# Optimization experiments

Measured on AMD Instinct MI355X. Metric: run time of the kernel, lower is better.

## Reference

```python
import jax, jax.numpy as jnp
import numpy as np

B, D_IN, N, K, L, D_OUT = 64, 1024, 50000, 32, 3, 256


def setup_inputs() -> dict:
    key = jax.random.key(0)
    k = jax.random.split(key, 7)
    x = jax.random.normal(k[0], (B, D_IN), dtype=jnp.float32)
    W0 = jax.random.normal(k[1], (N, D_IN), dtype=jnp.float32) * 0.02
    b0 = jax.random.normal(k[2], (N,), dtype=jnp.float32) * 0.02
    Wv = jax.random.normal(k[3], (L, N, K), dtype=jnp.float32) * 0.1
    Wout = jax.random.normal(k[4], (D_OUT, N), dtype=jnp.float32) * 0.02
    bout = jax.random.normal(k[5], (D_OUT,), dtype=jnp.float32) * 0.02
    src = jax.random.randint(k[6], (L, N, K), 0, N, dtype=jnp.int64)
    return {"x": x, "W0": W0, "b0": b0, "Wv": Wv, "Wout": Wout, "bout": bout, "src": src}


def reference(x, W0, b0, Wv, Wout, bout, src):
    # layer 0: dense input->sources, relu, transpose -> [N, B]
    h = jax.nn.relu(x @ W0.T + b0).T

    # each hidden layer: per-vertex gather of K source activations + 1xK matmul + relu
    def step(h_prev, layer):
        w, s = layer                      # w: [N, K], s: [N, K]
        gathered = h_prev[s]              # [N, K, B] irregular gather
        h_new = jax.nn.relu(jnp.einsum('nk,nkb->nb', w, gathered))
        return h_new, None

    h, _ = jax.lax.scan(step, h, (Wv, src))

    # last layer -> output Linear (the module's _linear_dummy)
    return h.T @ Wout.T + bout            # [B, D_OUT]
```

## Files before the change

### kernel.cpp

```cpp
#include <hip/hip_runtime.h>

#define NV 50000
#define NVP 50176
#define BDIM 64
#define DIN 1024
#define KFAN 32
#define DOUT 256
#define KSTEPS (DIN / 32)
#define OPC_CHUNK 128
#define OPC_NCH (NVP / OPC_CHUNK)

typedef short bf16x8 __attribute__((ext_vector_type(8)));
typedef float f32x4 __attribute__((ext_vector_type(4)));

__device__ __forceinline__ unsigned short bf16_rtn(float f) {
  unsigned u = __float_as_uint(f);
  return (unsigned short)((u + 0x7fffu + ((u >> 16) & 1u)) >> 16);
}
__device__ __forceinline__ float bf16_to_f(unsigned short v) {
  return __uint_as_float(((unsigned)v) << 16);
}

__global__ __launch_bounds__(256) void pack_x(const float* __restrict__ x,
                                              uint4* __restrict__ xpk) {
  int tid = blockIdx.x * 256 + threadIdx.x;
  int ks = tid >> 8;
  int g = (tid >> 6) & 3;
  int l = tid & 63;
  int b = g * 16 + (l & 15);
  int k0 = ks * 32 + (l >> 4) * 8;
  unsigned hi[8], lo[8];
#pragma unroll
  for (int j = 0; j < 8; ++j) {
    float f = x[b * DIN + k0 + j];
    unsigned u = __float_as_uint(f);
    hi[j] = u >> 16;
    float fh = __uint_as_float(u & 0xffff0000u);
    lo[j] = bf16_rtn(f - fh);
  }
  uint4 vh, vl;
  vh.x = hi[0] | (hi[1] << 16); vh.y = hi[2] | (hi[3] << 16);
  vh.z = hi[4] | (hi[5] << 16); vh.w = hi[6] | (hi[7] << 16);
  vl.x = lo[0] | (lo[1] << 16); vl.y = lo[2] | (lo[3] << 16);
  vl.z = lo[4] | (lo[5] << 16); vl.w = lo[6] | (lo[7] << 16);
  xpk[(ks * 4 + g) * 128 + l] = vh;
  xpk[(ks * 4 + g) * 128 + 64 + l] = vl;
}

__global__ __launch_bounds__(64) void layer0_mfma(
    const float* __restrict__ W0, const float* __restrict__ b0,
    const uint4* __restrict__ xpk, unsigned short* __restrict__ h)
{
  const int lane = threadIdx.x;
  const int n_base = blockIdx.x * 16;
  const int rq = lane >> 4;
  const int rr = lane & 15;

  const float* wp = W0 + (size_t)(n_base + rr) * DIN + rq * 8;

  f32x4 acc[4];
#pragma unroll
  for (int g = 0; g < 4; ++g) acc[g] = (f32x4){0.f, 0.f, 0.f, 0.f};

  float4 wc0 = *(const float4*)(wp);
  float4 wc1 = *(const float4*)(wp + 4);
  uint4 xc[4][2];
#pragma unroll
  for (int g = 0; g < 4; ++g) {
    xc[g][0] = xpk[g * 128 + lane];
    xc[g][1] = xpk[g * 128 + 64 + lane];
  }

  for (int ks = 0; ks < KSTEPS; ++ks) {
    float4 wn0, wn1;
    uint4 xn[4][2];
    if (ks + 1 < KSTEPS) {
      const int ko = (ks + 1) * 32;
      wn0 = *(const float4*)(wp + ko);
      wn1 = *(const float4*)(wp + ko + 4);
      const int xb = (ks + 1) * 512;
#pragma unroll
      for (int g = 0; g < 4; ++g) {
        xn[g][0] = xpk[xb + g * 128 + lane];
        xn[g][1] = xpk[xb + g * 128 + 64 + lane];
      }
    }
    bf16x8 whi, wlo;
    {
      float wf[8] = {wc0.x, wc0.y, wc0.z, wc0.w, wc1.x, wc1.y, wc1.z, wc1.w};
#pragma unroll
      for (int e = 0; e < 8; ++e) {
        unsigned u = __float_as_uint(wf[e]);
        whi[e] = (short)(u >> 16);
        float l = wf[e] - __uint_as_float(u & 0xffff0000u);
        wlo[e] = (short)bf16_rtn(l);
      }
    }
#pragma unroll
    for (int g = 0; g < 4; ++g) {
      bf16x8 xh = __builtin_bit_cast(bf16x8, xc[g][0]);
      bf16x8 xl = __builtin_bit_cast(bf16x8, xc[g][1]);
      acc[g] = __builtin_amdgcn_mfma_f32_16x16x32_bf16(whi, xh, acc[g], 0, 0, 0);
      acc[g] = __builtin_amdgcn_mfma_f32_16x16x32_bf16(wlo, xh, acc[g], 0, 0, 0);
      acc[g] = __builtin_amdgcn_mfma_f32_16x16x32_bf16(whi, xl, acc[g], 0, 0, 0);
    }
    if (ks + 1 < KSTEPS) {
      wc0 = wn0; wc1 = wn1;
#pragma unroll
      for (int g = 0; g < 4; ++g) { xc[g][0] = xn[g][0]; xc[g][1] = xn[g][1]; }
    }
  }

#pragma unroll
  for (int r = 0; r < 4; ++r) {
    int n = n_base + rq * 4 + r;
    float bias = b0[n];
#pragma unroll
    for (int g = 0; g < 4; ++g) {
      float v = fmaxf(acc[g][r] + bias, 0.f);
      h[(size_t)n * BDIM + g * 16 + rr] = bf16_rtn(v);
    }
  }
}

__global__ __launch_bounds__(256) void sparse_layer(
    const unsigned short* __restrict__ hin, const float* __restrict__ wv,
    const int* __restrict__ src, unsigned short* __restrict__ hout)
{
  const int lane = threadIdx.x & 63;
  int n = blockIdx.x * 4 + (threadIdx.x >> 6);
  n = __builtin_amdgcn_readfirstlane(n);
  const float* wrow = wv + (size_t)n * KFAN;
  const int* srow = src + (size_t)n * KFAN;
  float acc = 0.f;
#pragma unroll
  for (int k = 0; k < KFAN; ++k) {
    int s = srow[k];
    float w = wrow[k];
    acc = fmaf(w, bf16_to_f(hin[(size_t)s * BDIM + lane]), acc);
  }
  hout[(size_t)n * BDIM + lane] = bf16_rtn(fmaxf(acc, 0.f));
}

__global__ __launch_bounds__(256) void transpose_h(
    const unsigned short* __restrict__ h, unsigned short* __restrict__ hT)
{
  const int lane = threadIdx.x & 63;
  const int wv = threadIdx.x >> 6;
  const int n0 = (blockIdx.x * 4 + wv) * 8;
  unsigned short v[8];
#pragma unroll
  for (int i = 0; i < 8; ++i) {
    int n = n0 + i;
    v[i] = (n < NV) ? h[(size_t)n * BDIM + lane] : (unsigned short)0;
  }
  uint4 o;
  o.x = v[0] | ((unsigned)v[1] << 16);
  o.y = v[2] | ((unsigned)v[3] << 16);
  o.z = v[4] | ((unsigned)v[5] << 16);
  o.w = v[6] | ((unsigned)v[7] << 16);
  *(uint4*)(hT + (size_t)lane * NVP + n0) = o;
}

__global__ __launch_bounds__(64) void out_partial_mfma(
    const unsigned short* __restrict__ hT, const float* __restrict__ Wout,
    float* __restrict__ part)
{
  const int lane = threadIdx.x;
  const int rq = lane >> 4;
  const int rr = lane & 15;
  const int dtile = blockIdx.x;
  const int chunk = blockIdx.y;

  f32x4 acc[4][4];
#pragma unroll
  for (int f = 0; f < 4; ++f)
#pragma unroll
    for (int g = 0; g < 4; ++g) acc[f][g] = (f32x4){0.f, 0.f, 0.f, 0.f};

#pragma unroll
  for (int ks = 0; ks < OPC_CHUNK / 32; ++ks) {
    const int n0 = chunk * OPC_CHUNK + ks * 32 + rq * 8;
    bf16x8 hb[4];
#pragma unroll
    for (int g = 0; g < 4; ++g)
      hb[g] = *(const bf16x8*)(hT + (size_t)(g * 16 + rr) * NVP + n0);
    int nb = n0 > (NV - 8) ? (NV - 8) : n0;
#pragma unroll
    for (int f = 0; f < 4; ++f) {
      const float* wp = Wout + (size_t)(dtile * 64 + f * 16 + rr) * NV + nb;
      float4 a0 = *(const float4*)(wp);
      float4 a1 = *(const float4*)(wp + 4);
      float wf[8] = {a0.x, a0.y, a0.z, a0.w, a1.x, a1.y, a1.z, a1.w};
      bf16x8 whi, wlo;
#pragma unroll
      for (int e = 0; e < 8; ++e) {
        unsigned u = __float_as_uint(wf[e]);
        whi[e] = (short)(u >> 16);
        float l = wf[e] - __uint_as_float(u & 0xffff0000u);
        wlo[e] = (short)bf16_rtn(l);
      }
#pragma unroll
      for (int g = 0; g < 4; ++g) {
        acc[f][g] = __builtin_amdgcn_mfma_f32_16x16x32_bf16(whi, hb[g], acc[f][g], 0, 0, 0);
        acc[f][g] = __builtin_amdgcn_mfma_f32_16x16x32_bf16(wlo, hb[g], acc[f][g], 0, 0, 0);
      }
    }
  }
  float* pbase = part + ((size_t)dtile * OPC_NCH + chunk) * 4096;
#pragma unroll
  for (int f = 0; f < 4; ++f)
#pragma unroll
    for (int g = 0; g < 4; ++g)
#pragma unroll
      for (int r = 0; r < 4; ++r)
        pbase[(f * 16 + rq * 4 + r) * 64 + g * 16 + rr] = acc[f][g][r];
}

__global__ __launch_bounds__(256) void out_reduce(
    const float* __restrict__ part, const float* __restrict__ bout,
    float* __restrict__ out)
{
  int tid = blockIdx.x * 256 + threadIdx.x;
  int b = tid & 63;
  int d = tid >> 6;
  int dtile = d >> 6;
  int dd = d & 63;
  float s = bout[d];
  for (int c = 0; c < OPC_NCH; ++c)
    s += part[((size_t)dtile * OPC_NCH + c) * 4096 + dd * 64 + b];
  out[(size_t)b * DOUT + d] = s;
}

extern "C" void kernel_launch(void* const* d_in, const int* in_sizes, int n_in,
                              void* d_out, int out_size, void* d_ws, size_t ws_size,
                              hipStream_t stream)
{
  const float* x    = (const float*)d_in[0];
  const float* W0   = (const float*)d_in[1];
  const float* b0   = (const float*)d_in[2];
  const float* Wv   = (const float*)d_in[3];
  const float* Wout = (const float*)d_in[4];
  const float* bout = (const float*)d_in[5];
  const int*   src  = (const int*)d_in[6];
  float* out = (float*)d_out;

  char* ws = (char*)d_ws;
  const size_t hbf = (size_t)NV * BDIM * 2;
  const size_t hTb = (size_t)NVP * BDIM * 2;
  unsigned short* hb0 = (unsigned short*)ws;
  unsigned short* hb1 = (unsigned short*)(ws + hbf);
  unsigned short* hT  = (unsigned short*)(ws + 2 * hbf);
  uint4* xpk  = (uint4*)(ws + 2 * hbf + hTb);
  float* part = (float*)(ws + 2 * hbf + hTb);

  pack_x<<<32, 256, 0, stream>>>(x, xpk);
  layer0_mfma<<<NV / 16, 64, 0, stream>>>(W0, b0, xpk, hb0);

  const size_t lstride = (size_t)NV * KFAN;
  sparse_layer<<<NV / 4, 256, 0, stream>>>(hb0, Wv, src, hb1);
  sparse_layer<<<NV / 4, 256, 0, stream>>>(hb1, Wv + lstride, src + lstride, hb0);
  sparse_layer<<<NV / 4, 256, 0, stream>>>(hb0, Wv + 2 * lstride, src + 2 * lstride, hb1);

  transpose_h<<<NVP / 32, 256, 0, stream>>>(hb1, hT);
  out_partial_mfma<<<dim3(4, OPC_NCH), 64, 0, stream>>>(hT, Wout, part);
  out_reduce<<<(BDIM * DOUT) / 256, 256, 0, stream>>>(part, bout, out);
}
```

Measured before the change: 202.6 us.

## Stage W0 tiles via async global-to-LDS loads with swizzle in layer0

Rewrites layer0 so each 256-thread block handles 64 rows and streams W0 32-column slices into double-buffered shared memory using global_load_lds with an XOR swizzle, instead of each wave loading its rows directly into registers. The goal is coalesced 128-byte row segments, fewer VGPRs for prefetch, and overlap of the next slice's load with the current MFMAs. It adds a __syncthreads per k-step, bounds clamping for the last partial block, and now reloads the packed x from global every iteration rather than prefetching it.

```diff
diff --git a/kernel.cpp b/kernel.cpp
--- a/kernel.cpp
+++ b/kernel.cpp
@@ -20,6 +20,11 @@
 __device__ __forceinline__ float bf16_to_f(unsigned short v) {
   return __uint_as_float(((unsigned)v) << 16);
 }
+__device__ __forceinline__ void gload_lds16(const float* g, float* l) {
+  __builtin_amdgcn_global_load_lds(
+      (const __attribute__((address_space(1))) void*)g,
+      (__attribute__((address_space(3))) void*)l, 16, 0, 0);
+}
 
 __global__ __launch_bounds__(256) void pack_x(const float* __restrict__ x,
                                               uint4* __restrict__ xpk) {
@@ -47,47 +52,63 @@
   xpk[(ks * 4 + g) * 128 + 64 + l] = vl;
 }
 
-__global__ __launch_bounds__(64) void layer0_mfma(
+__global__ __launch_bounds__(256) void layer0_mfma(
     const float* __restrict__ W0, const float* __restrict__ b0,
     const uint4* __restrict__ xpk, unsigned short* __restrict__ h)
 {
-  const int lane = threadIdx.x;
-  const int n_base = blockIdx.x * 16;
+  __shared__ float wlds[2][64 * 32];
+  const int t = threadIdx.x;
+  const int lane = t & 63;
+  const int w = t >> 6;
   const int rq = lane >> 4;
   const int rr = lane & 15;
-
-  const float* wp = W0 + (size_t)(n_base + rr) * DIN + rq * 8;
+  const int n0 = blockIdx.x * 64;
+
+  int s_row[2], s_srcg[2];
+#pragma unroll
+  for (int p = 0; p < 2; ++p) {
+    int flat = p * 256 + t;
+    s_row[p] = flat >> 3;
+    s_srcg[p] = (flat & 7) ^ (s_row[p] & 7);
+  }
+  int rowg0 = n0 + s_row[0]; if (rowg0 > NV - 1) rowg0 = NV - 1;
+  int rowg1 = n0 + s_row[1]; if (rowg1 > NV - 1) rowg1 = NV - 1;
+  const float* sp0 = W0 + (size_t)rowg0 * DIN + s_srcg[0] * 4;
+  const float* sp1 = W0 + (size_t)rowg1 * DIN + s_srcg[1] * 4;
+
+  const int myrow = w * 16 + rr;
+  const int sw = (myrow & 7) << 4;
+  const int off0 = (myrow * 128 + ((rq * 32) ^ sw)) >> 2;
+  const int off1 = (myrow * 128 + ((rq * 32 + 16) ^ sw)) >> 2;
 
   f32x4 acc[4];
 #pragma unroll
   for (int g = 0; g < 4; ++g) acc[g] = (f32x4){0.f, 0.f, 0.f, 0.f};
 
-  float4 wc0 = *(const float4*)(wp);
-  float4 wc1 = *(const float4*)(wp + 4);
-  uint4 xc[4][2];
-#pragma unroll
-  for (int g = 0; g < 4; ++g) {
-    xc[g][0] = xpk[g * 128 + lane];
-    xc[g][1] = xpk[g * 128 + 64 + lane];
-  }
+  gload_lds16(sp0, &wlds[0][(0 * 256 + t) * 4]);
+  gload_lds16(sp1, &wlds[0][(1 * 256 + t) * 4]);
+  __syncthreads();
 
   for (int ks = 0; ks < KSTEPS; ++ks) {
-    float4 wn0, wn1;
-    uint4 xn[4][2];
+    const int cur = ks & 1;
     if (ks + 1 < KSTEPS) {
       const int ko = (ks + 1) * 32;
-      wn0 = *(const float4*)(wp + ko);
-      wn1 = *(const float4*)(wp + ko + 4);
-      const int xb = (ks + 1) * 512;
-#pragma unroll
-      for (int g = 0; g < 4; ++g) {
-        xn[g][0] = xpk[xb + g * 128 + lane];
-        xn[g][1] = xpk[xb + g * 128 + 64 + lane];
-      }
-    }
+      gload_lds16(sp0 + ko, &wlds[cur ^ 1][(0 * 256 + t) * 4]);
+      gload_lds16(sp1 + ko, &wlds[cur ^ 1][(1 * 256 + t) * 4]);
+    }
+    const int xb = ks * 512;
+    uint4 xc[4][2];
+#pragma unroll
+    for (int g = 0; g < 4; ++g) {
+      xc[g][0] = xpk[xb + g * 128 + lane];
+      xc[g][1] = xpk[xb + g * 128 + 64 + lane];
+    }
+    const float* wb = &wlds[cur][0];
+    float4 wv0 = *(const float4*)(wb + off0);
+    float4 wv1 = *(const float4*)(wb + off1);
     bf16x8 whi, wlo;
     {
-      float wf[8] = {wc0.x, wc0.y, wc0.z, wc0.w, wc1.x, wc1.y, wc1.z, wc1.w};
+      float wf[8] = {wv0.x, wv0.y, wv0.z, wv0.w, wv1.x, wv1.y, wv1.z, wv1.w};
 #pragma unroll
       for (int e = 0; e < 8; ++e) {
         unsigned u = __float_as_uint(wf[e]);
@@ -104,21 +125,19 @@
       acc[g] = __builtin_amdgcn_mfma_f32_16x16x32_bf16(wlo, xh, acc[g], 0, 0, 0);
       acc[g] = __builtin_amdgcn_mfma_f32_16x16x32_bf16(whi, xl, acc[g], 0, 0, 0);
     }
-    if (ks + 1 < KSTEPS) {
-      wc0 = wn0; wc1 = wn1;
-#pragma unroll
-      for (int g = 0; g < 4; ++g) { xc[g][0] = xn[g][0]; xc[g][1] = xn[g][1]; }
-    }
+    __syncthreads();
   }
 
 #pragma unroll
   for (int r = 0; r < 4; ++r) {
-    int n = n_base + rq * 4 + r;
-    float bias = b0[n];
-#pragma unroll
-    for (int g = 0; g < 4; ++g) {
-      float v = fmaxf(acc[g][r] + bias, 0.f);
-      h[(size_t)n * BDIM + g * 16 + rr] = bf16_rtn(v);
+    int n = n0 + w * 16 + rq * 4 + r;
+    if (n < NV) {
+      float bias = b0[n];
+#pragma unroll
+      for (int g = 0; g < 4; ++g) {
+        float v = fmaxf(acc[g][r] + bias, 0.f);
+        h[(size_t)n * BDIM + g * 16 + rr] = bf16_rtn(v);
+      }
     }
   }
 }
@@ -255,7 +274,7 @@
   float* part = (float*)(ws + 2 * hbf + hTb);
 
   pack_x<<<32, 256, 0, stream>>>(x, xpk);
-  layer0_mfma<<<NV / 16, 64, 0, stream>>>(W0, b0, xpk, hb0);
+  layer0_mfma<<<(NV + 63) / 64, 256, 0, stream>>>(W0, b0, xpk, hb0);
 
   const size_t lstride = (size_t)NV * KFAN;
   sparse_layer<<<NV / 4, 256, 0, stream>>>(hb0, Wv, src, hb1);
```

After: 202.4 us. No clear change (-0.1%).
